# Optimization experiments

Measured on AMD Instinct MI355X. Metric: run time of the kernel, lower is better.

## Reference

```python
import jax, jax.numpy as jnp
import numpy as np

H = 8  # head_num

def setup_inputs() -> dict:
    key = jax.random.key(0)
    k1, k2, k3, k4, k5 = jax.random.split(key, 5)
    n, e = 4096, 128
    x = jax.random.normal(k1, (n, e), dtype=jnp.float32)
    # torch Linear weights stored here as [in, out]; scale ~ 1/sqrt(fan_in)
    w_qkv = jax.random.normal(k2, (e, e * 3 * H), dtype=jnp.float32) * (1.0 / np.sqrt(e))
    b_qkv = jax.random.normal(k3, (e * 3 * H,), dtype=jnp.float32) * 0.01
    w_proj = jax.random.normal(k4, (e * H, e), dtype=jnp.float32) * (1.0 / np.sqrt(e * H))
    b_proj = jax.random.normal(k5, (e,), dtype=jnp.float32) * 0.01
    return {"x": x, "w_qkv": w_qkv, "b_qkv": b_qkv, "w_proj": w_proj, "b_proj": b_proj}

def reference(x, w_qkv, b_qkv, w_proj, b_proj):
    n, e = x.shape
    # packed layout along output dim is (h, d, qkv) per rearrange 'n (h d qkv) -> qkv h n d'
    qkv = (x @ w_qkv + b_qkv).reshape(n, H, e, 3)          # [n, h, d, 3]
    q = jnp.transpose(qkv[..., 0], (1, 0, 2))              # [h, n, d]
    k = jnp.transpose(qkv[..., 1], (1, 0, 2))
    v = jnp.transpose(qkv[..., 2], (1, 0, 2))
    energy = jnp.einsum('hqd,hkd->hqk', q, k)              # [h, n, n]
    scaling = jnp.asarray(e, x.dtype) ** 0.5
    att = jax.nn.softmax(energy, axis=-1) / scaling        # post-softmax scale (as in source)
    out = jnp.einsum('hqk,hkd->hqd', att, v)               # [h, n, d]
    out = jnp.transpose(out, (1, 0, 2)).reshape(n, H * e)  # [n, h*d]
    return out @ w_proj + b_proj
```

## Files before the change

kernel.cpp:

```cpp
#include <hip/hip_runtime.h>
#include <hip/hip_fp16.h>


#define N_TOK 4096
#define DH 128
#define NH 8

#define EXP2F(x) __builtin_amdgcn_exp2f(x)

typedef _Float16 f16;
typedef __attribute__((ext_vector_type(8))) _Float16 f16x8;
typedef __attribute__((ext_vector_type(2))) __fp16 hf2;
typedef __attribute__((ext_vector_type(4))) __fp16 hf4;
typedef __attribute__((ext_vector_type(4))) float f32x4;

#define GLD16(gsrc, ldst) __builtin_amdgcn_global_load_lds( \
    (const __attribute__((address_space(1))) void*)(gsrc), \
    (__attribute__((address_space(3))) void*)(ldst), 16, 0, 0)

__global__ __launch_bounds__(256) void conv_weights(
    const float* __restrict__ w_proj, const float* __restrict__ w_qkv,
    const float* __restrict__ b_qkv, const float* __restrict__ x,
    f16* __restrict__ wpT, f16* __restrict__ wqkvT, float* __restrict__ bperm,
    f16* __restrict__ xh)
{
  int t = blockIdx.x * 256 + threadIdx.x;
  if (t < 131072) {
    int k = t >> 7, col = t & 127;
    wpT[col * 1024 + k] = (f16)w_proj[t];
  } else if (t < 524288) {
    t -= 131072;
    int k = t / 3072;
    int col = t - k * 3072;
    int hh = col / 384;
    int rem = col - hh * 384;
    int d = rem / 3;
    int s = rem - d * 3;
    int colp = s * 1024 + hh * 128 + d;
    float scale = (s == 0) ? 1.4426950408889634f : 1.0f;
    wqkvT[colp * 128 + k] = (f16)(w_qkv[t] * scale);
    if (k == 0) bperm[colp] = b_qkv[col] * scale;
  } else {
    t -= 524288;
    xh[t] = (f16)x[t];
  }
}

__global__ __launch_bounds__(256) void qkv_gemm2(
    const f16* __restrict__ xh, const f16* __restrict__ wqkvT,
    const float* __restrict__ bperm,
    f16* __restrict__ Qh, f16* __restrict__ Kh, f16* __restrict__ Vt)
{
  const int cb = blockIdx.x;
  const int rb = blockIdx.y;
  const int tid = threadIdx.x;
  const int w = tid >> 6, lane = tid & 63;
  const int l16 = lane & 15, lhi = lane >> 4;
  const int s = cb >> 3, h = cb & 7;

  f16x8 xf[2][4];
#pragma unroll
  for (int m = 0; m < 2; ++m)
#pragma unroll
    for (int kt = 0; kt < 4; ++kt)
      xf[m][kt] = *(const f16x8*)(xh +
          (size_t)(rb * 128 + w * 32 + m * 16 + l16) * 128 + kt * 32 + lhi * 8);

  f32x4 acc[8][2];
#pragma unroll
  for (int nt = 0; nt < 8; ++nt)
#pragma unroll
    for (int m = 0; m < 2; ++m) acc[nt][m] = (f32x4){0.f, 0.f, 0.f, 0.f};

#pragma unroll
  for (int nt = 0; nt < 8; ++nt)
#pragma unroll
    for (int kt = 0; kt < 4; ++kt) {
      f16x8 wf = *(const f16x8*)(wqkvT + (size_t)(cb * 128 + nt * 16 + l16) * 128 + kt * 32 + lhi * 8);
      acc[nt][0] = __builtin_amdgcn_mfma_f32_16x16x32_f16(wf, xf[0][kt], acc[nt][0], 0, 0, 0);
      acc[nt][1] = __builtin_amdgcn_mfma_f32_16x16x32_f16(wf, xf[1][kt], acc[nt][1], 0, 0, 0);
    }

#pragma unroll
  for (int nt = 0; nt < 8; ++nt) {
    f32x4 bb = *(const f32x4*)(bperm + cb * 128 + nt * 16 + 4 * lhi);
#pragma unroll
    for (int m = 0; m < 2; ++m) acc[nt][m] += bb;
  }

  if (s == 2) {
#pragma unroll
    for (int nt = 0; nt < 8; ++nt)
#pragma unroll
      for (int m = 0; m < 2; ++m)
#pragma unroll
        for (int r = 0; r < 4; ++r)
          Vt[(size_t)(h * 128 + nt * 16 + 4 * lhi + r) * N_TOK + rb * 128 + w * 32 + m * 16 + l16] =
              (f16)acc[nt][m][r];
  } else {
    __shared__ f16 tr[128][136];
#pragma unroll
    for (int nt = 0; nt < 8; ++nt)
#pragma unroll
      for (int m = 0; m < 2; ++m)
#pragma unroll
        for (int r = 0; r < 4; ++r)
          tr[w * 32 + m * 16 + l16][nt * 16 + 4 * lhi + r] = (f16)acc[nt][m][r];
    __syncthreads();
    f16* dst = (s == 0 ? Qh : Kh) + (size_t)(h * N_TOK + rb * 128) * 128;
    int r = tid >> 1, dh = (tid & 1) * 64;
#pragma unroll
    for (int i = 0; i < 8; ++i)
      *(f16x8*)(dst + r * 128 + dh + i * 8) = *(const f16x8*)(&tr[r][dh + i * 8]);
  }
}

__global__ __launch_bounds__(256, 3) void flash_attn(
    const f16* __restrict__ Qh, const f16* __restrict__ Kh,
    const f16* __restrict__ Vt, f16* __restrict__ opart, float* __restrict__ mlpart)
{
  const int bid = blockIdx.x;
  const int h = bid & 7;
  const int rem8 = bid >> 3;
  const int sp = rem8 % 3, qb = rem8 / 3;
  const int tid = threadIdx.x;
  const int w = tid >> 6, lane = tid & 63;
  const int l16 = lane & 15, lhi = lane >> 4;

  __shared__ __align__(16) char smem[32768];

  f16x8 qf[2][4];
#pragma unroll
  for (int m = 0; m < 2; ++m)
#pragma unroll
    for (int kt = 0; kt < 4; ++kt)
      qf[m][kt] = *(const f16x8*)(Qh +
          (size_t)(h * N_TOK + qb * 128 + w * 32 + m * 16 + l16) * DH + kt * 32 + lhi * 8);

  int koff[4][4], voff[2][8];
#pragma unroll
  for (int nt = 0; nt < 4; ++nt) {
    int row = 32 * (nt >> 1) + 8 * (l16 >> 2) + 4 * (nt & 1) + (l16 & 3);
    int fk = (row & 3) | ((row & 8) >> 1);
#pragma unroll
    for (int kt = 0; kt < 4; ++kt)
      koff[nt][kt] = row * 256 + ((kt * 4 + lhi) ^ fk) * 16;
  }
#pragma unroll
  for (int ks = 0; ks < 2; ++ks)
#pragma unroll
    for (int dt = 0; dt < 8; ++dt) {
      int rowv = dt * 16 + l16;
      voff[ks][dt] = rowv * 128 + (((ks * 4 + lhi) ^ (rowv & 7))) * 16;
    }

  f32x4 o[2][8];
#pragma unroll
  for (int m = 0; m < 2; ++m)
#pragma unroll
    for (int dt = 0; dt < 8; ++dt) o[m][dt] = (f32x4){0.f, 0.f, 0.f, 0.f};
  float mrun[2] = {-3e38f, -3e38f}, lrun[2] = {0.f, 0.f};

  const int kb0 = (sp * 64) / 3;
  const int kb1 = ((sp + 1) * 64) / 3;

  const f16* kp[4];
  const f16* vp[4];
#pragma unroll
  for (int c4 = 0; c4 < 4; ++c4) {
    int c = w * 4 + c4;
    int row = c * 4 + (lane >> 4);
    int fk = (row & 3) | ((row & 8) >> 1);
    kp[c4] = Kh + (size_t)h * N_TOK * DH + (size_t)(kb0 * 64 + row) * DH + ((lane & 15) ^ fk) * 8;
    int rowv = c * 8 + (lane >> 3);
    vp[c4] = Vt + (size_t)h * DH * N_TOK + (size_t)rowv * N_TOK + kb0 * 64 + ((lane & 7) ^ (rowv & 7)) * 8;
  }

  const char* kd = smem;
  const char* vd = smem + 16384;

  for (int kb = kb0; kb < kb1; ++kb) {
#pragma unroll
    for (int c4 = 0; c4 < 4; ++c4) {
      int c = w * 4 + c4;
      GLD16(kp[c4], (char*)smem + c * 1024);
      GLD16(vp[c4], (char*)smem + 16384 + c * 1024);
      kp[c4] += 64 * DH;
      vp[c4] += 64;
    }
    __syncthreads();

    f32x4 sv[2][4];
    __builtin_amdgcn_s_setprio(1);
#pragma unroll
    for (int nt = 0; nt < 4; ++nt) {
      f32x4 a0 = {0.f, 0.f, 0.f, 0.f}, a1 = {0.f, 0.f, 0.f, 0.f};
#pragma unroll
      for (int kt = 0; kt < 4; ++kt) {
        f16x8 kf = *(const f16x8*)(kd + koff[nt][kt]);
        a0 = __builtin_amdgcn_mfma_f32_16x16x32_f16(kf, qf[0][kt], a0, 0, 0, 0);
        a1 = __builtin_amdgcn_mfma_f32_16x16x32_f16(kf, qf[1][kt], a1, 0, 0, 0);
      }
      sv[0][nt] = a0; sv[1][nt] = a1;
    }
    __builtin_amdgcn_s_setprio(0);

    f16x8 pf[2][2];
#pragma unroll
    for (int m = 0; m < 2; ++m) {
      f32x4 mv;
#pragma unroll
      for (int r = 0; r < 4; ++r)
        mv[r] = fmaxf(fmaxf(sv[m][0][r], sv[m][1][r]), fmaxf(sv[m][2][r], sv[m][3][r]));
      float pmax = fmaxf(fmaxf(mv[0], mv[1]), fmaxf(mv[2], mv[3]));
      if (!__all(pmax - mrun[m] <= 8.f)) {
        float rm = fmaxf(pmax, __shfl_xor(pmax, 16));
        rm = fmaxf(rm, __shfl_xor(rm, 32));
        float mnew = fmaxf(mrun[m], rm);
        float sc = EXP2F(mrun[m] - mnew);
        lrun[m] *= sc;
#pragma unroll
        for (int dt = 0; dt < 8; ++dt) o[m][dt] *= sc;
        mrun[m] = mnew;
      }
      float mr = mrun[m];
      f32x4 ps = {0.f, 0.f, 0.f, 0.f};
#pragma unroll
      for (int nt = 0; nt < 4; ++nt)
#pragma unroll
        for (int r = 0; r < 4; ++r) {
          float p = EXP2F(sv[m][nt][r] - mr);
          sv[m][nt][r] = p;
          ps[r] += p;
        }
      lrun[m] += (ps[0] + ps[1]) + (ps[2] + ps[3]);
#pragma unroll
      for (int ks = 0; ks < 2; ++ks) {
        union { f16x8 v; hf2 hh[4]; } u;
        u.hh[0] = __builtin_amdgcn_cvt_pkrtz(sv[m][2 * ks][0], sv[m][2 * ks][1]);
        u.hh[1] = __builtin_amdgcn_cvt_pkrtz(sv[m][2 * ks][2], sv[m][2 * ks][3]);
        u.hh[2] = __builtin_amdgcn_cvt_pkrtz(sv[m][2 * ks + 1][0], sv[m][2 * ks + 1][1]);
        u.hh[3] = __builtin_amdgcn_cvt_pkrtz(sv[m][2 * ks + 1][2], sv[m][2 * ks + 1][3]);
        pf[m][ks] = u.v;
      }
    }

    __builtin_amdgcn_s_setprio(1);
#pragma unroll
    for (int ks = 0; ks < 2; ++ks)
#pragma unroll
      for (int dt = 0; dt < 8; ++dt) {
        f16x8 vf = *(const f16x8*)(vd + voff[ks][dt]);
        o[0][dt] = __builtin_amdgcn_mfma_f32_16x16x32_f16(vf, pf[0][ks], o[0][dt], 0, 0, 0);
        o[1][dt] = __builtin_amdgcn_mfma_f32_16x16x32_f16(vf, pf[1][ks], o[1][dt], 0, 0, 0);
      }
    __builtin_amdgcn_s_setprio(0);

    __syncthreads();
  }

  f16* ob = opart + ((size_t)((sp * 8 + h) * 32 + qb)) * 16384;
  float* mlb = mlpart + ((size_t)((sp * 8 + h) * 32 + qb)) * 256;
#pragma unroll
  for (int m = 0; m < 2; ++m) {
    float lr = lrun[m];
    lr += __shfl_xor(lr, 16);
    lr += __shfl_xor(lr, 32);
    float rl = 1.0f / lr;
    int n = w * 32 + m * 16 + l16;
#pragma unroll
    for (int dt = 0; dt < 8; ++dt) {
      union { hf4 v; hf2 h[2]; } u;
      u.h[0] = __builtin_amdgcn_cvt_pkrtz(o[m][dt][0] * rl, o[m][dt][1] * rl);
      u.h[1] = __builtin_amdgcn_cvt_pkrtz(o[m][dt][2] * rl, o[m][dt][3] * rl);
      *(hf4*)(ob + (size_t)n * 128 + dt * 16 + 4 * lhi) = u.v;
    }
    if (lhi == 0) {
      mlb[n] = mrun[m];
      mlb[128 + n] = lr;
    }
  }
}

__global__ __launch_bounds__(256) void proj_combine(
    const f16* __restrict__ opart, const float* __restrict__ mlpart,
    const f16* __restrict__ wpT, const float* __restrict__ b_proj,
    float* __restrict__ out)
{
  const int tid = threadIdx.x;
  const int w = tid >> 6;
  const int lane = tid & 63;
  const int l16 = lane & 15, lhi = lane >> 4;
  const int rb = blockIdx.x * 16;
  const int qb = rb >> 7;
  const int nl0 = rb & 127;

  __shared__ f16 A[16][1032];
  __shared__ float wl[8][16][3];

  const float isc = 0.08838834764831845f;
  if (tid < 128) {
    int hh = tid >> 4, n = tid & 15;
    float mi[3], li[3];
#pragma unroll
    for (int i = 0; i < 3; ++i) {
      const float* ml = mlpart + ((size_t)((i * 8 + hh) * 32 + qb)) * 256 + nl0 + n;
      mi[i] = ml[0]; li[i] = ml[128];
    }
    float mt = fmaxf(fmaxf(mi[0], mi[1]), mi[2]);
    float ni[3], tot = 0.f;
#pragma unroll
    for (int i = 0; i < 3; ++i) { ni[i] = EXP2F(mi[i] - mt) * li[i]; tot += ni[i]; }
    float rl = isc / tot;
#pragma unroll
    for (int i = 0; i < 3; ++i) wl[hh][n][i] = ni[i] * rl;
  }
  __syncthreads();

  {
    int n = tid & 15, c = tid >> 4;
    int hh = c >> 1, d0 = (c & 1) * 64;
    size_t roff = (size_t)(nl0 + n) * 128 + d0;
    const f16* O0 = opart + ((size_t)((0 + hh) * 32 + qb)) * 16384 + roff;
    const f16* O1 = opart + ((size_t)((8 + hh) * 32 + qb)) * 16384 + roff;
    const f16* O2 = opart + ((size_t)((16 + hh) * 32 + qb)) * 16384 + roff;
    float w0 = wl[hh][n][0], w1 = wl[hh][n][1], w2 = wl[hh][n][2];
#pragma unroll
    for (int j = 0; j < 8; ++j) {
      f16x8 a0 = *(const f16x8*)(O0 + j * 8);
      f16x8 a1 = *(const f16x8*)(O1 + j * 8);
      f16x8 a2 = *(const f16x8*)(O2 + j * 8);
      f16x8 res;
#pragma unroll
      for (int e = 0; e < 8; ++e)
        res[e] = (f16)((float)a0[e] * w0 + (float)a1[e] * w1 + (float)a2[e] * w2);
      *(f16x8*)(&A[n][hh * 128 + d0 + j * 8]) = res;
    }
  }
  __syncthreads();

  f32x4 o[2];
  o[0] = (f32x4){0.f, 0.f, 0.f, 0.f};
  o[1] = (f32x4){0.f, 0.f, 0.f, 0.f};

#pragma unroll
  for (int kb = 0; kb < 32; ++kb) {
    int k0 = kb * 32 + lhi * 8;
    f16x8 a = *(const f16x8*)(&A[l16][k0]);
#pragma unroll
    for (int dtl = 0; dtl < 2; ++dtl) {
      int dt = w * 2 + dtl;
      f16x8 b = *(const f16x8*)(wpT + (size_t)(dt * 16 + l16) * 1024 + k0);
      o[dtl] = __builtin_amdgcn_mfma_f32_16x16x32_f16(a, b, o[dtl], 0, 0, 0);
    }
  }

#pragma unroll
  for (int dtl = 0; dtl < 2; ++dtl) {
    int col = (w * 2 + dtl) * 16 + l16;
    float bp = b_proj[col];
#pragma unroll
    for (int r = 0; r < 4; ++r)
      out[(size_t)(rb + lhi * 4 + r) * 128 + col] = o[dtl][r] + bp;
  }
}

extern "C" void kernel_launch(void* const* d_in, const int* in_sizes, int n_in,
                              void* d_out, int out_size, void* d_ws, size_t ws_size,
                              hipStream_t stream) {
  const float* x      = (const float*)d_in[0];
  const float* w_qkv  = (const float*)d_in[1];
  const float* b_qkv  = (const float*)d_in[2];
  const float* w_proj = (const float*)d_in[3];
  const float* b_proj = (const float*)d_in[4];
  float* out = (float*)d_out;

  char* ws = (char*)d_ws;
  const size_t MB = 1024 * 1024;
  f16*   Qh     = (f16*)(ws);
  f16*   Kh     = (f16*)(ws + 8 * MB);
  f16*   Vt     = (f16*)(ws + 16 * MB);
  f16*   opart  = (f16*)(ws + 24 * MB);
  float* mlpart = (float*)(ws + 48 * MB);
  f16*   wpT    = (f16*)(ws + 49 * MB);
  f16*   wqkvT  = (f16*)(ws + 49 * MB + 256 * 1024);
  float* bperm  = (float*)(ws + 50 * MB);
  f16*   xh     = (f16*)(ws + 50 * MB + 256 * 1024);

  hipLaunchKernelGGL(conv_weights, dim3(4096), dim3(256), 0, stream,
                     w_proj, w_qkv, b_qkv, x, wpT, wqkvT, bperm, xh);
  hipLaunchKernelGGL(qkv_gemm2, dim3(24, 32), dim3(256), 0, stream,
                     xh, wqkvT, bperm, Qh, Kh, Vt);
  hipLaunchKernelGGL(flash_attn, dim3(768), dim3(256), 0, stream,
                     Qh, Kh, Vt, opart, mlpart);
  hipLaunchKernelGGL(proj_combine, dim3(256), dim3(256), 0, stream,
                     opart, mlpart, wpT, b_proj, out);
}
```

Baseline: 127.5 us.

## Use 128-key tiles and 2-way KV split in flash attention

The attention kernel now stages 128 keys per iteration into a 64KB LDS buffer and processes them as two 64-key halves, halving the number of barriers per key. The KV range is split two ways instead of three, so the grid shrinks from 768 to 512 blocks and the combine step merges two partials. The intent is to cut synchronisation and partial-combine overhead. The cost is lower occupancy (launch bounds drop to 2 blocks per CU, more LDS per block) and fewer blocks to spread across the 256 CUs.

```diff
diff --git a/kernel.cpp b/kernel.cpp
--- a/kernel.cpp
+++ b/kernel.cpp
@@ -115,19 +115,17 @@
   }
 }
 
-__global__ __launch_bounds__(256, 3) void flash_attn(
+__global__ __launch_bounds__(256, 2) void flash_attn(
     const f16* __restrict__ Qh, const f16* __restrict__ Kh,
     const f16* __restrict__ Vt, f16* __restrict__ opart, float* __restrict__ mlpart)
 {
   const int bid = blockIdx.x;
-  const int h = bid & 7;
-  const int rem8 = bid >> 3;
-  const int sp = rem8 % 3, qb = rem8 / 3;
+  const int h = bid & 7, sp = (bid >> 3) & 1, qb = bid >> 4;
   const int tid = threadIdx.x;
   const int w = tid >> 6, lane = tid & 63;
   const int l16 = lane & 15, lhi = lane >> 4;
 
-  __shared__ __align__(16) char smem[32768];
+  __shared__ __align__(16) char smem[65536];
 
   f16x8 qf[2][4];
 #pragma unroll
@@ -151,7 +149,8 @@
 #pragma unroll
     for (int dt = 0; dt < 8; ++dt) {
       int rowv = dt * 16 + l16;
-      voff[ks][dt] = rowv * 128 + (((ks * 4 + lhi) ^ (rowv & 7))) * 16;
+      int fk = (rowv & 3) | ((rowv & 8) >> 1);
+      voff[ks][dt] = rowv * 256 + (((ks * 4 + lhi) ^ fk)) * 16;
     }
 
   f32x4 o[2][8];
@@ -161,100 +160,106 @@
     for (int dt = 0; dt < 8; ++dt) o[m][dt] = (f32x4){0.f, 0.f, 0.f, 0.f};
   float mrun[2] = {-3e38f, -3e38f}, lrun[2] = {0.f, 0.f};
 
-  const int kb0 = (sp * 64) / 3;
-  const int kb1 = ((sp + 1) * 64) / 3;
-
-  const f16* kp[4];
-  const f16* vp[4];
-#pragma unroll
-  for (int c4 = 0; c4 < 4; ++c4) {
-    int c = w * 4 + c4;
-    int row = c * 4 + (lane >> 4);
-    int fk = (row & 3) | ((row & 8) >> 1);
-    kp[c4] = Kh + (size_t)h * N_TOK * DH + (size_t)(kb0 * 64 + row) * DH + ((lane & 15) ^ fk) * 8;
-    int rowv = c * 8 + (lane >> 3);
-    vp[c4] = Vt + (size_t)h * DH * N_TOK + (size_t)rowv * N_TOK + kb0 * 64 + ((lane & 7) ^ (rowv & 7)) * 8;
-  }
+  const f16* Kgh = Kh + (size_t)h * N_TOK * DH;
+  const f16* Vgh = Vt + (size_t)h * DH * N_TOK;
+
+  auto stage = [&](int kb) {
+#pragma unroll
+    for (int c8 = 0; c8 < 8; ++c8) {
+      int c = w * 8 + c8;
+      int row = c * 4 + (lane >> 4);
+      int fk = (row & 3) | ((row & 8) >> 1);
+      int chunk = (lane & 15) ^ fk;
+      {
+        const f16* src = Kgh + (size_t)(kb * 128 + row) * DH + chunk * 8;
+        GLD16(src, (char*)smem + c * 1024);
+      }
+      {
+        const f16* src = Vgh + (size_t)row * N_TOK + kb * 128 + chunk * 8;
+        GLD16(src, (char*)smem + 32768 + c * 1024);
+      }
+    }
+  };
 
   const char* kd = smem;
-  const char* vd = smem + 16384;
-
-  for (int kb = kb0; kb < kb1; ++kb) {
-#pragma unroll
-    for (int c4 = 0; c4 < 4; ++c4) {
-      int c = w * 4 + c4;
-      GLD16(kp[c4], (char*)smem + c * 1024);
-      GLD16(vp[c4], (char*)smem + 16384 + c * 1024);
-      kp[c4] += 64 * DH;
-      vp[c4] += 64;
-    }
+  const char* vd = smem + 32768;
+  const int kb0 = sp * 16;
+
+  for (int kb = kb0; kb < kb0 + 16; ++kb) {
+    stage(kb);
     __syncthreads();
 
-    f32x4 sv[2][4];
-    __builtin_amdgcn_s_setprio(1);
-#pragma unroll
-    for (int nt = 0; nt < 4; ++nt) {
-      f32x4 a0 = {0.f, 0.f, 0.f, 0.f}, a1 = {0.f, 0.f, 0.f, 0.f};
-#pragma unroll
-      for (int kt = 0; kt < 4; ++kt) {
-        f16x8 kf = *(const f16x8*)(kd + koff[nt][kt]);
-        a0 = __builtin_amdgcn_mfma_f32_16x16x32_f16(kf, qf[0][kt], a0, 0, 0, 0);
-        a1 = __builtin_amdgcn_mfma_f32_16x16x32_f16(kf, qf[1][kt], a1, 0, 0, 0);
+#pragma unroll
+    for (int half = 0; half < 2; ++half) {
+      const int kadd = half * 16384;
+      const int vadd = half * 128;
+
+      f32x4 sv[2][4];
+      __builtin_amdgcn_s_setprio(1);
+#pragma unroll
+      for (int nt = 0; nt < 4; ++nt) {
+        f32x4 a0 = {0.f, 0.f, 0.f, 0.f}, a1 = {0.f, 0.f, 0.f, 0.f};
+#pragma unroll
+        for (int kt = 0; kt < 4; ++kt) {
+          f16x8 kf = *(const f16x8*)(kd + kadd + koff[nt][kt]);
+          a0 = __builtin_amdgcn_mfma_f32_16x16x32_f16(kf, qf[0][kt], a0, 0, 0, 0);
+          a1 = __builtin_amdgcn_mfma_f32_16x16x32_f16(kf, qf[1][kt], a1, 0, 0, 0);
+        }
+        sv[0][nt] = a0; sv[1][nt] = a1;
       }
-      sv[0][nt] = a0; sv[1][nt] = a1;
-    }
-    __builtin_amdgcn_s_setprio(0);
-
-    f16x8 pf[2][2];
-#pragma unroll
-    for (int m = 0; m < 2; ++m) {
-      f32x4 mv;
-#pragma unroll
-      for (int r = 0; r < 4; ++r)
-        mv[r] = fmaxf(fmaxf(sv[m][0][r], sv[m][1][r]), fmaxf(sv[m][2][r], sv[m][3][r]));
-      float pmax = fmaxf(fmaxf(mv[0], mv[1]), fmaxf(mv[2], mv[3]));
-      if (!__all(pmax - mrun[m] <= 8.f)) {
-        float rm = fmaxf(pmax, __shfl_xor(pmax, 16));
-        rm = fmaxf(rm, __shfl_xor(rm, 32));
-        float mnew = fmaxf(mrun[m], rm);
-        float sc = EXP2F(mrun[m] - mnew);
-        lrun[m] *= sc;
-#pragma unroll
-        for (int dt = 0; dt < 8; ++dt) o[m][dt] *= sc;
-        mrun[m] = mnew;
+      __builtin_amdgcn_s_setprio(0);
+
+      f16x8 pf[2][2];
+#pragma unroll
+      for (int m = 0; m < 2; ++m) {
+        f32x4 mv;
+#pragma unroll
+        for (int r = 0; r < 4; ++r)
+          mv[r] = fmaxf(fmaxf(sv[m][0][r], sv[m][1][r]), fmaxf(sv[m][2][r], sv[m][3][r]));
+        float pmax = fmaxf(fmaxf(mv[0], mv[1]), fmaxf(mv[2], mv[3]));
+        if (!__all(pmax - mrun[m] <= 8.f)) {
+          float rm = fmaxf(pmax, __shfl_xor(pmax, 16));
+          rm = fmaxf(rm, __shfl_xor(rm, 32));
+          float mnew = fmaxf(mrun[m], rm);
+          float sc = EXP2F(mrun[m] - mnew);
+          lrun[m] *= sc;
+#pragma unroll
+          for (int dt = 0; dt < 8; ++dt) o[m][dt] *= sc;
+          mrun[m] = mnew;
+        }
+        float mr = mrun[m];
+        f32x4 ps = {0.f, 0.f, 0.f, 0.f};
+#pragma unroll
+        for (int nt = 0; nt < 4; ++nt)
+#pragma unroll
+          for (int r = 0; r < 4; ++r) {
+            float p = EXP2F(sv[m][nt][r] - mr);
+            sv[m][nt][r] = p;
+            ps[r] += p;
+          }
+        lrun[m] += (ps[0] + ps[1]) + (ps[2] + ps[3]);
+#pragma unroll
+        for (int ks = 0; ks < 2; ++ks) {
+          union { f16x8 v; hf2 hh[4]; } u;
+          u.hh[0] = __builtin_amdgcn_cvt_pkrtz(sv[m][2 * ks][0], sv[m][2 * ks][1]);
+          u.hh[1] = __builtin_amdgcn_cvt_pkrtz(sv[m][2 * ks][2], sv[m][2 * ks][3]);
+          u.hh[2] = __builtin_amdgcn_cvt_pkrtz(sv[m][2 * ks + 1][0], sv[m][2 * ks + 1][1]);
+          u.hh[3] = __builtin_amdgcn_cvt_pkrtz(sv[m][2 * ks + 1][2], sv[m][2 * ks + 1][3]);
+          pf[m][ks] = u.v;
+        }
       }
-      float mr = mrun[m];
-      f32x4 ps = {0.f, 0.f, 0.f, 0.f};
-#pragma unroll
-      for (int nt = 0; nt < 4; ++nt)
-#pragma unroll
-        for (int r = 0; r < 4; ++r) {
-          float p = EXP2F(sv[m][nt][r] - mr);
-          sv[m][nt][r] = p;
-          ps[r] += p;
+
+      __builtin_amdgcn_s_setprio(1);
+#pragma unroll
+      for (int ks = 0; ks < 2; ++ks)
+#pragma unroll
+        for (int dt = 0; dt < 8; ++dt) {
+          f16x8 vf = *(const f16x8*)(vd + vadd + voff[ks][dt]);
+          o[0][dt] = __builtin_amdgcn_mfma_f32_16x16x32_f16(vf, pf[0][ks], o[0][dt], 0, 0, 0);
+          o[1][dt] = __builtin_amdgcn_mfma_f32_16x16x32_f16(vf, pf[1][ks], o[1][dt], 0, 0, 0);
         }
-      lrun[m] += (ps[0] + ps[1]) + (ps[2] + ps[3]);
-#pragma unroll
-      for (int ks = 0; ks < 2; ++ks) {
-        union { f16x8 v; hf2 hh[4]; } u;
-        u.hh[0] = __builtin_amdgcn_cvt_pkrtz(sv[m][2 * ks][0], sv[m][2 * ks][1]);
-        u.hh[1] = __builtin_amdgcn_cvt_pkrtz(sv[m][2 * ks][2], sv[m][2 * ks][3]);
-        u.hh[2] = __builtin_amdgcn_cvt_pkrtz(sv[m][2 * ks + 1][0], sv[m][2 * ks + 1][1]);
-        u.hh[3] = __builtin_amdgcn_cvt_pkrtz(sv[m][2 * ks + 1][2], sv[m][2 * ks + 1][3]);
-        pf[m][ks] = u.v;
-      }
-    }
-
-    __builtin_amdgcn_s_setprio(1);
-#pragma unroll
-    for (int ks = 0; ks < 2; ++ks)
-#pragma unroll
-      for (int dt = 0; dt < 8; ++dt) {
-        f16x8 vf = *(const f16x8*)(vd + voff[ks][dt]);
-        o[0][dt] = __builtin_amdgcn_mfma_f32_16x16x32_f16(vf, pf[0][ks], o[0][dt], 0, 0, 0);
-        o[1][dt] = __builtin_amdgcn_mfma_f32_16x16x32_f16(vf, pf[1][ks], o[1][dt], 0, 0, 0);
-      }
-    __builtin_amdgcn_s_setprio(0);
+      __builtin_amdgcn_s_setprio(0);
+    }
 
     __syncthreads();
   }
@@ -296,24 +301,19 @@
   const int nl0 = rb & 127;
 
   __shared__ f16 A[16][1032];
-  __shared__ float wl[8][16][3];
+  __shared__ float wl[8][16][2];
 
   const float isc = 0.08838834764831845f;
   if (tid < 128) {
     int hh = tid >> 4, n = tid & 15;
-    float mi[3], li[3];
-#pragma unroll
-    for (int i = 0; i < 3; ++i) {
-      const float* ml = mlpart + ((size_t)((i * 8 + hh) * 32 + qb)) * 256 + nl0 + n;
-      mi[i] = ml[0]; li[i] = ml[128];
-    }
-    float mt = fmaxf(fmaxf(mi[0], mi[1]), mi[2]);
-    float ni[3], tot = 0.f;
-#pragma unroll
-    for (int i = 0; i < 3; ++i) { ni[i] = EXP2F(mi[i] - mt) * li[i]; tot += ni[i]; }
-    float rl = isc / tot;
-#pragma unroll
-    for (int i = 0; i < 3; ++i) wl[hh][n][i] = ni[i] * rl;
+    const float* ml0 = mlpart + ((size_t)((0 + hh) * 32 + qb)) * 256 + nl0 + n;
+    const float* ml1 = mlpart + ((size_t)((8 + hh) * 32 + qb)) * 256 + nl0 + n;
+    float m0 = ml0[0], l0 = ml0[128], m1 = ml1[0], l1 = ml1[128];
+    float mt = fmaxf(m0, m1);
+    float n0 = EXP2F(m0 - mt) * l0, n1 = EXP2F(m1 - mt) * l1;
+    float rl = isc / (n0 + n1);
+    wl[hh][n][0] = n0 * rl;
+    wl[hh][n][1] = n1 * rl;
   }
   __syncthreads();
 
@@ -323,17 +323,15 @@
     size_t roff = (size_t)(nl0 + n) * 128 + d0;
     const f16* O0 = opart + ((size_t)((0 + hh) * 32 + qb)) * 16384 + roff;
     const f16* O1 = opart + ((size_t)((8 + hh) * 32 + qb)) * 16384 + roff;
-    const f16* O2 = opart + ((size_t)((16 + hh) * 32 + qb)) * 16384 + roff;
-    float w0 = wl[hh][n][0], w1 = wl[hh][n][1], w2 = wl[hh][n][2];
+    float w0 = wl[hh][n][0], w1 = wl[hh][n][1];
 #pragma unroll
     for (int j = 0; j < 8; ++j) {
       f16x8 a0 = *(const f16x8*)(O0 + j * 8);
       f16x8 a1 = *(const f16x8*)(O1 + j * 8);
-      f16x8 a2 = *(const f16x8*)(O2 + j * 8);
       f16x8 res;
 #pragma unroll
       for (int e = 0; e < 8; ++e)
-        res[e] = (f16)((float)a0[e] * w0 + (float)a1[e] * w1 + (float)a2[e] * w2);
+        res[e] = (f16)((float)a0[e] * w0 + (float)a1[e] * w1);
       *(f16x8*)(&A[n][hh * 128 + d0 + j * 8]) = res;
     }
   }
@@ -381,17 +379,17 @@
   f16*   Kh     = (f16*)(ws + 8 * MB);
   f16*   Vt     = (f16*)(ws + 16 * MB);
   f16*   opart  = (f16*)(ws + 24 * MB);
-  float* mlpart = (float*)(ws + 48 * MB);
-  f16*   wpT    = (f16*)(ws + 49 * MB);
-  f16*   wqkvT  = (f16*)(ws + 49 * MB + 256 * 1024);
-  float* bperm  = (float*)(ws + 50 * MB);
-  f16*   xh     = (f16*)(ws + 50 * MB + 256 * 1024);
+  float* mlpart = (float*)(ws + 40 * MB);
+  f16*   wpT    = (f16*)(ws + 40 * MB + 512 * 1024);
+  f16*   wqkvT  = (f16*)(ws + 40 * MB + 768 * 1024);
+  float* bperm  = (float*)(ws + 41 * MB + 512 * 1024);
+  f16*   xh     = (f16*)(ws + 41 * MB + 768 * 1024);
 
   hipLaunchKernelGGL(conv_weights, dim3(4096), dim3(256), 0, stream,
                      w_proj, w_qkv, b_qkv, x, wpT, wqkvT, bperm, xh);
   hipLaunchKernelGGL(qkv_gemm2, dim3(24, 32), dim3(256), 0, stream,
                      xh, wqkvT, bperm, Qh, Kh, Vt);
-  hipLaunchKernelGGL(flash_attn, dim3(768), dim3(256), 0, stream,
+  hipLaunchKernelGGL(flash_attn, dim3(512), dim3(256), 0, stream,
                      Qh, Kh, Vt, opart, mlpart);
   hipLaunchKernelGGL(proj_combine, dim3(256), dim3(256), 0, stream,
                      opart, mlpart, wpT, b_proj, out);
```

After: 123.0 us. 3.6% less time.

## Split attention keys into four chunks and fuse x fp16 conversion into QKV GEMM

Applied to the files above, without the earlier changes.

The flash attention split-K factor goes from 3 to 4. That gives 1024 blocks with equal 16-tile chunks and raises the launch bound to 4 blocks per CU, and the combine kernel now merges four partial softmax states. The separate fp32-to-fp16 conversion pass over x is removed: the QKV GEMM loads fp32 x directly and converts it in registers. This cuts one global round-trip and shrinks the conversion launch. In exchange, combine traffic and partial-output storage grow, and register pressure under the tighter occupancy bound may cause spills.

```diff
diff --git a/kernel.cpp b/kernel.cpp
--- a/kernel.cpp
+++ b/kernel.cpp
@@ -20,15 +20,14 @@
 
 __global__ __launch_bounds__(256) void conv_weights(
     const float* __restrict__ w_proj, const float* __restrict__ w_qkv,
-    const float* __restrict__ b_qkv, const float* __restrict__ x,
-    f16* __restrict__ wpT, f16* __restrict__ wqkvT, float* __restrict__ bperm,
-    f16* __restrict__ xh)
+    const float* __restrict__ b_qkv,
+    f16* __restrict__ wpT, f16* __restrict__ wqkvT, float* __restrict__ bperm)
 {
   int t = blockIdx.x * 256 + threadIdx.x;
   if (t < 131072) {
     int k = t >> 7, col = t & 127;
     wpT[col * 1024 + k] = (f16)w_proj[t];
-  } else if (t < 524288) {
+  } else {
     t -= 131072;
     int k = t / 3072;
     int col = t - k * 3072;
@@ -40,14 +39,11 @@
     float scale = (s == 0) ? 1.4426950408889634f : 1.0f;
     wqkvT[colp * 128 + k] = (f16)(w_qkv[t] * scale);
     if (k == 0) bperm[colp] = b_qkv[col] * scale;
-  } else {
-    t -= 524288;
-    xh[t] = (f16)x[t];
   }
 }
 
 __global__ __launch_bounds__(256) void qkv_gemm2(
-    const f16* __restrict__ xh, const f16* __restrict__ wqkvT,
+    const float* __restrict__ x, const f16* __restrict__ wqkvT,
     const float* __restrict__ bperm,
     f16* __restrict__ Qh, f16* __restrict__ Kh, f16* __restrict__ Vt)
 {
@@ -62,9 +58,14 @@
 #pragma unroll
   for (int m = 0; m < 2; ++m)
 #pragma unroll
-    for (int kt = 0; kt < 4; ++kt)
-      xf[m][kt] = *(const f16x8*)(xh +
-          (size_t)(rb * 128 + w * 32 + m * 16 + l16) * 128 + kt * 32 + lhi * 8);
+    for (int kt = 0; kt < 4; ++kt) {
+      const float* xp = x + (size_t)(rb * 128 + w * 32 + m * 16 + l16) * 128 + kt * 32 + lhi * 8;
+      f32x4 x0 = *(const f32x4*)xp, x1 = *(const f32x4*)(xp + 4);
+      f16x8 v;
+#pragma unroll
+      for (int j = 0; j < 4; ++j) { v[j] = (f16)x0[j]; v[4 + j] = (f16)x1[j]; }
+      xf[m][kt] = v;
+    }
 
   f32x4 acc[8][2];
 #pragma unroll
@@ -115,14 +116,14 @@
   }
 }
 
-__global__ __launch_bounds__(256, 3) void flash_attn(
+__global__ __launch_bounds__(256, 4) void flash_attn(
     const f16* __restrict__ Qh, const f16* __restrict__ Kh,
     const f16* __restrict__ Vt, f16* __restrict__ opart, float* __restrict__ mlpart)
 {
   const int bid = blockIdx.x;
   const int h = bid & 7;
-  const int rem8 = bid >> 3;
-  const int sp = rem8 % 3, qb = rem8 / 3;
+  const int sp = (bid >> 3) & 3;
+  const int qb = bid >> 5;
   const int tid = threadIdx.x;
   const int w = tid >> 6, lane = tid & 63;
   const int l16 = lane & 15, lhi = lane >> 4;
@@ -161,8 +162,7 @@
     for (int dt = 0; dt < 8; ++dt) o[m][dt] = (f32x4){0.f, 0.f, 0.f, 0.f};
   float mrun[2] = {-3e38f, -3e38f}, lrun[2] = {0.f, 0.f};
 
-  const int kb0 = (sp * 64) / 3;
-  const int kb1 = ((sp + 1) * 64) / 3;
+  const int kb0 = sp * 16;
 
   const f16* kp[4];
   const f16* vp[4];
@@ -179,7 +179,7 @@
   const char* kd = smem;
   const char* vd = smem + 16384;
 
-  for (int kb = kb0; kb < kb1; ++kb) {
+  for (int it = 0; it < 16; ++it) {
 #pragma unroll
     for (int c4 = 0; c4 < 4; ++c4) {
       int c = w * 4 + c4;
@@ -296,24 +296,24 @@
   const int nl0 = rb & 127;
 
   __shared__ f16 A[16][1032];
-  __shared__ float wl[8][16][3];
+  __shared__ float wl[8][16][4];
 
   const float isc = 0.08838834764831845f;
   if (tid < 128) {
     int hh = tid >> 4, n = tid & 15;
-    float mi[3], li[3];
-#pragma unroll
-    for (int i = 0; i < 3; ++i) {
+    float mi[4], li[4];
+#pragma unroll
+    for (int i = 0; i < 4; ++i) {
       const float* ml = mlpart + ((size_t)((i * 8 + hh) * 32 + qb)) * 256 + nl0 + n;
       mi[i] = ml[0]; li[i] = ml[128];
     }
-    float mt = fmaxf(fmaxf(mi[0], mi[1]), mi[2]);
-    float ni[3], tot = 0.f;
-#pragma unroll
-    for (int i = 0; i < 3; ++i) { ni[i] = EXP2F(mi[i] - mt) * li[i]; tot += ni[i]; }
+    float mt = fmaxf(fmaxf(mi[0], mi[1]), fmaxf(mi[2], mi[3]));
+    float ni[4], tot = 0.f;
+#pragma unroll
+    for (int i = 0; i < 4; ++i) { ni[i] = EXP2F(mi[i] - mt) * li[i]; tot += ni[i]; }
     float rl = isc / tot;
 #pragma unroll
-    for (int i = 0; i < 3; ++i) wl[hh][n][i] = ni[i] * rl;
+    for (int i = 0; i < 4; ++i) wl[hh][n][i] = ni[i] * rl;
   }
   __syncthreads();
 
@@ -324,16 +324,19 @@
     const f16* O0 = opart + ((size_t)((0 + hh) * 32 + qb)) * 16384 + roff;
     const f16* O1 = opart + ((size_t)((8 + hh) * 32 + qb)) * 16384 + roff;
     const f16* O2 = opart + ((size_t)((16 + hh) * 32 + qb)) * 16384 + roff;
-    float w0 = wl[hh][n][0], w1 = wl[hh][n][1], w2 = wl[hh][n][2];
+    const f16* O3 = opart + ((size_t)((24 + hh) * 32 + qb)) * 16384 + roff;
+    float w0 = wl[hh][n][0], w1 = wl[hh][n][1], w2 = wl[hh][n][2], w3 = wl[hh][n][3];
 #pragma unroll
     for (int j = 0; j < 8; ++j) {
       f16x8 a0 = *(const f16x8*)(O0 + j * 8);
       f16x8 a1 = *(const f16x8*)(O1 + j * 8);
       f16x8 a2 = *(const f16x8*)(O2 + j * 8);
+      f16x8 a3 = *(const f16x8*)(O3 + j * 8);
       f16x8 res;
 #pragma unroll
       for (int e = 0; e < 8; ++e)
-        res[e] = (f16)((float)a0[e] * w0 + (float)a1[e] * w1 + (float)a2[e] * w2);
+        res[e] = (f16)((float)a0[e] * w0 + (float)a1[e] * w1
+                     + (float)a2[e] * w2 + (float)a3[e] * w3);
       *(f16x8*)(&A[n][hh * 128 + d0 + j * 8]) = res;
     }
   }
@@ -381,17 +384,16 @@
   f16*   Kh     = (f16*)(ws + 8 * MB);
   f16*   Vt     = (f16*)(ws + 16 * MB);
   f16*   opart  = (f16*)(ws + 24 * MB);
-  float* mlpart = (float*)(ws + 48 * MB);
-  f16*   wpT    = (f16*)(ws + 49 * MB);
-  f16*   wqkvT  = (f16*)(ws + 49 * MB + 256 * 1024);
-  float* bperm  = (float*)(ws + 50 * MB);
-  f16*   xh     = (f16*)(ws + 50 * MB + 256 * 1024);
-
-  hipLaunchKernelGGL(conv_weights, dim3(4096), dim3(256), 0, stream,
-                     w_proj, w_qkv, b_qkv, x, wpT, wqkvT, bperm, xh);
+  float* mlpart = (float*)(ws + 56 * MB);
+  f16*   wpT    = (f16*)(ws + 57 * MB);
+  f16*   wqkvT  = (f16*)(ws + 57 * MB + 256 * 1024);
+  float* bperm  = (float*)(ws + 58 * MB);
+
+  hipLaunchKernelGGL(conv_weights, dim3(2048), dim3(256), 0, stream,
+                     w_proj, w_qkv, b_qkv, wpT, wqkvT, bperm);
   hipLaunchKernelGGL(qkv_gemm2, dim3(24, 32), dim3(256), 0, stream,
-                     xh, wqkvT, bperm, Qh, Kh, Vt);
-  hipLaunchKernelGGL(flash_attn, dim3(768), dim3(256), 0, stream,
+                     x, wqkvT, bperm, Qh, Kh, Vt);
+  hipLaunchKernelGGL(flash_attn, dim3(1024), dim3(256), 0, stream,
                      Qh, Kh, Vt, opart, mlpart);
   hipLaunchKernelGGL(proj_combine, dim3(256), dim3(256), 0, stream,
                      opart, mlpart, wpT, b_proj, out);
```

Result: slower. 291.7 us (+128.8%).
